# Kernel tuning notes

Hardware: AMD Instinct MI355X
Metric: run time of the kernel (lower is better)

## Reference

```python
import jax, jax.numpy as jnp
import numpy as np

B, C, H, W = 4, 64, 128, 128
KH, KW = 5, 5
PAD = 2
HEADS, DIM_HEAD = 8, 8


def setup_inputs() -> dict:
    key = jax.random.key(0)
    k1, k2, k3, k4 = jax.random.split(key, 4)
    return {
        "features1": jax.random.normal(k1, (B, C, H, W), dtype=jnp.float32),
        "features2": jax.random.normal(k2, (B, C, H, W), dtype=jnp.float32),
        "rel_h": jax.random.normal(k3, (C // 2, 1, 1, KH, 1), dtype=jnp.float32),
        "rel_w": jax.random.normal(k4, (C // 2, 1, 1, 1, KW), dtype=jnp.float32),
    }


def reference(features1, features2, rel_h, rel_w):
    b, c, h, w = features1.shape
    K = KH * KW
    # pad key/value source spatially
    padded = jnp.pad(features2, ((0, 0), (0, 0), (PAD, PAD), (PAD, PAD)))
    # materialize sliding windows: [B, C, H, W, KH*KW], kw index minor (matches torch unfold(2).unfold(3))
    windows = jnp.stack(
        [padded[:, :, i:i + h, j:j + w] for i in range(KH) for j in range(KW)],
        axis=-1,
    )
    # relative position bias: first C/2 channels get rel_h, last C/2 get rel_w
    relh = jnp.broadcast_to(rel_h.reshape(c // 2, KH, 1), (c // 2, KH, KW))
    relw = jnp.broadcast_to(rel_w.reshape(c // 2, 1, KW), (c // 2, KH, KW))
    rel = jnp.concatenate([relh, relw], axis=0).reshape(c, K)  # [C, K]
    k = windows + rel[None, :, None, None, :]
    v = windows
    q = features1.reshape(b, HEADS, DIM_HEAD, h, w, 1)
    k = k.reshape(b, HEADS, DIM_HEAD, h, w, K)
    v = v.reshape(b, HEADS, DIM_HEAD, h, w, K)
    # per-channel windowed softmax attention (no reduction over channel in scores)
    attn = jax.nn.softmax(q * k, axis=-1)
    # einsum 'abcdef,abcdef->acbde' from torch: output is [B, dim_head, heads, H, W]
    out = jnp.einsum('bhcxyk,bhcxyk->bchxy', attn, v)
    return out.reshape(b, c, h, w)
```

## Files before the change

### kernel.cpp

```cpp
#include <hip/hip_runtime.h>

#define B_ 4
#define C_ 64
#define H_ 128
#define W_ 128
#define R_ 4
#define NROWS (R_ + 4)
#define LOG2E 1.44269504088896340736f

template<int HALF>
__device__ __forceinline__ void sa_body(int x, int y0,
    const float* __restrict__ f1p, const float* __restrict__ f2p,
    const float* __restrict__ relp, float* __restrict__ outp)
{
    float rel5[5];
    #pragma unroll
    for (int k = 0; k < 5; ++k) rel5[k] = relp[k];

    int coff[5]; float msk[5];
    #pragma unroll
    for (int j = 0; j < 5; ++j) {
        const int kx = x + j - 2;
        coff[j] = kx < 0 ? 0 : (kx > W_ - 1 ? W_ - 1 : kx);
        msk[j]  = (kx >= 0 && kx < W_) ? 1.0f : 0.0f;
    }

    float w[NROWS][5];
    #pragma unroll
    for (int t = 0; t < NROWS; ++t) {
        const int ky = y0 + t - 2;
        if (ky >= 0 && ky < H_) {
            const float* rp = f2p + ky * W_;
            #pragma unroll
            for (int j = 0; j < 5; ++j) w[t][j] = rp[coff[j]];
        } else {
            #pragma unroll
            for (int j = 0; j < 5; ++j) w[t][j] = 0.0f;
        }
    }
    float qv[R_];
    #pragma unroll
    for (int r = 0; r < R_; ++r) qv[r] = f1p[(y0 + r) * W_ + x];

    #pragma unroll
    for (int t = 0; t < NROWS; ++t) {
        #pragma unroll
        for (int j = 0; j < 5; ++j) w[t][j] *= msk[j];
    }

    #pragma unroll
    for (int r = 0; r < R_; ++r) {
        const float q2 = qv[r] * LOG2E;
        float prel[5];
        #pragma unroll
        for (int k = 0; k < 5; ++k) prel[k] = q2 * rel5[k];

        float sum0 = 0.f, sum1 = 0.f, dot0 = 0.f, dot1 = 0.f;
        #pragma unroll
        for (int i = 0; i < 5; ++i) {
            #pragma unroll
            for (int j = 0; j < 5; ++j) {
                const float v  = w[r + i][j];
                const float sc = __builtin_fmaf(q2, v, prel[HALF == 0 ? i : j]);
                const float p  = __builtin_amdgcn_exp2f(sc);
                if (((i * 5 + j) & 1) == 0) { sum0 += p; dot0 = __builtin_fmaf(p, v, dot0); }
                else                        { sum1 += p; dot1 = __builtin_fmaf(p, v, dot1); }
            }
        }
        const float sum = sum0 + sum1;
        const float dot = dot0 + dot1;
        outp[(y0 + r) * W_ + x] = dot * __builtin_amdgcn_rcpf(sum);
    }
}

__global__ __launch_bounds__(256) void sa_kernel(
    const float* __restrict__ f1, const float* __restrict__ f2,
    const float* __restrict__ relh, const float* __restrict__ relw,
    float* __restrict__ out)
{
    const int tid   = threadIdx.x;
    const int x     = tid & (W_ - 1);
    const int s     = tid >> 7;
    const int blk   = blockIdx.x;
    const int spair = blk & (H_ / R_ / 2 - 1);
    const int bc    = blk >> 4;
    const int c     = bc & (C_ - 1);
    const int b     = bc >> 6;
    const int y0    = __builtin_amdgcn_readfirstlane((spair * 2 + s) * R_);

    const size_t img = (size_t)(b * C_ + c) * (H_ * W_);
    const float* f1p = f1 + img;
    const float* f2p = f2 + img;

    const int c_out = (c & 7) * 8 + (c >> 3);
    float* outp = out + (size_t)(b * C_ + c_out) * (H_ * W_);

    if (c < C_ / 2) sa_body<0>(x, y0, f1p, f2p, relh + c * 5, outp);
    else            sa_body<1>(x, y0, f1p, f2p, relw + (c - C_ / 2) * 5, outp);
}

extern "C" void kernel_launch(void* const* d_in, const int* in_sizes, int n_in,
                              void* d_out, int out_size, void* d_ws, size_t ws_size,
                              hipStream_t stream) {
    const float* f1   = (const float*)d_in[0];
    const float* f2   = (const float*)d_in[1];
    const float* relh = (const float*)d_in[2];
    const float* relw = (const float*)d_in[3];
    float* out = (float*)d_out;

    const int grid = B_ * C_ * (H_ / R_ / 2);
    sa_kernel<<<grid, 256, 0, stream>>>(f1, f2, relh, relw, out);
}
```

Measured before the change: 24.93 us.

## Compute 4x4 output tile per thread with float4 loads and packed v2f math

Each thread now computes a 4-wide by 4-tall output tile instead of a 1-wide column of 4 rows. It loads f2 rows as three float4 vectors into a rotating 5-row register buffer, reads q with a float4 load and writes output with a float4 store. It also uses 2-wide vector FMA types that may map to packed FP32 instructions. The aim is to cut redundant window loads and per-element load instructions and raise ALU throughput. The cost is higher register pressure, and the grid shrinks to 1024 blocks.

```diff
diff --git a/kernel.cpp b/kernel.cpp
--- a/kernel.cpp
+++ b/kernel.cpp
@@ -4,12 +4,16 @@
 #define C_ 64
 #define H_ 128
 #define W_ 128
-#define R_ 4
-#define NROWS (R_ + 4)
 #define LOG2E 1.44269504088896340736f
 
+typedef float v2f __attribute__((ext_vector_type(2)));
+
+__device__ __forceinline__ v2f exp2v(v2f x) {
+    return (v2f){ __builtin_amdgcn_exp2f(x.x), __builtin_amdgcn_exp2f(x.y) };
+}
+
 template<int HALF>
-__device__ __forceinline__ void sa_body(int x, int y0,
+__device__ __forceinline__ void sa_body(int x0, int y0,
     const float* __restrict__ f1p, const float* __restrict__ f2p,
     const float* __restrict__ relp, float* __restrict__ outp)
 {
@@ -17,59 +21,93 @@
     #pragma unroll
     for (int k = 0; k < 5; ++k) rel5[k] = relp[k];
 
-    int coff[5]; float msk[5];
-    #pragma unroll
-    for (int j = 0; j < 5; ++j) {
-        const int kx = x + j - 2;
-        coff[j] = kx < 0 ? 0 : (kx > W_ - 1 ? W_ - 1 : kx);
-        msk[j]  = (kx >= 0 && kx < W_) ? 1.0f : 0.0f;
-    }
+    const float mL = (x0 > 0) ? 1.0f : 0.0f;
+    const float mR = (x0 < W_ - 4) ? 1.0f : 0.0f;
+    const int eM = (x0 >= 4) ? x0 - 4 : 0;
+    const int eC = x0;
+    const int eP = (x0 <= W_ - 8) ? x0 + 4 : W_ - 4;
 
-    float w[NROWS][5];
-    #pragma unroll
-    for (int t = 0; t < NROWS; ++t) {
-        const int ky = y0 + t - 2;
-        if (ky >= 0 && ky < H_) {
-            const float* rp = f2p + ky * W_;
-            #pragma unroll
-            for (int j = 0; j < 5; ++j) w[t][j] = rp[coff[j]];
-        } else {
-            #pragma unroll
-            for (int j = 0; j < 5; ++j) w[t][j] = 0.0f;
-        }
-    }
-    float qv[R_];
-    #pragma unroll
-    for (int r = 0; r < R_; ++r) qv[r] = f1p[(y0 + r) * W_ + x];
+    float w[5][8];
+
+    auto load_row = [&](int slot, int ky) {
+        const int kycl = ky < 0 ? 0 : (ky > H_ - 1 ? H_ - 1 : ky);
+        const float rv = ((unsigned)ky < (unsigned)H_) ? 1.0f : 0.0f;
+        const float* rp = f2p + kycl * W_;
+        const float4 qm = *(const float4*)(rp + eM);
+        const float4 q0 = *(const float4*)(rp + eC);
+        const float4 qp = *(const float4*)(rp + eP);
+        const float mLr = mL * rv, mRr = mR * rv;
+        w[slot][0] = qm.z * mLr; w[slot][1] = qm.w * mLr;
+        w[slot][2] = q0.x * rv;  w[slot][3] = q0.y * rv;
+        w[slot][4] = q0.z * rv;  w[slot][5] = q0.w * rv;
+        w[slot][6] = qp.x * mRr; w[slot][7] = qp.y * mRr;
+    };
 
     #pragma unroll
-    for (int t = 0; t < NROWS; ++t) {
-        #pragma unroll
-        for (int j = 0; j < 5; ++j) w[t][j] *= msk[j];
-    }
+    for (int t = 0; t < 4; ++t) load_row(t, y0 + t - 2);
 
     #pragma unroll
-    for (int r = 0; r < R_; ++r) {
-        const float q2 = qv[r] * LOG2E;
-        float prel[5];
+    for (int r = 0; r < 4; ++r) {
+        load_row((r + 4) % 5, y0 + r + 2);
+
+        const float4 q4 = *(const float4*)(f1p + (y0 + r) * W_ + x0);
+        const float qs[4] = {q4.x, q4.y, q4.z, q4.w};
+        float res[4];
+
         #pragma unroll
-        for (int k = 0; k < 5; ++k) prel[k] = q2 * rel5[k];
+        for (int xo = 0; xo < 4; ++xo) {
+            const float q2 = qs[xo] * LOG2E;
+            const v2f q2v = {q2, q2};
 
-        float sum0 = 0.f, sum1 = 0.f, dot0 = 0.f, dot1 = 0.f;
-        #pragma unroll
-        for (int i = 0; i < 5; ++i) {
+            float pr[5];
             #pragma unroll
-            for (int j = 0; j < 5; ++j) {
-                const float v  = w[r + i][j];
-                const float sc = __builtin_fmaf(q2, v, prel[HALF == 0 ? i : j]);
-                const float p  = __builtin_amdgcn_exp2f(sc);
-                if (((i * 5 + j) & 1) == 0) { sum0 += p; dot0 = __builtin_fmaf(p, v, dot0); }
-                else                        { sum1 += p; dot1 = __builtin_fmaf(p, v, dot1); }
+            for (int k = 0; k < 5; ++k) pr[k] = q2 * rel5[k];
+            const v2f prA = {pr[0], pr[1]};
+            const v2f prB = {pr[2], pr[3]};
+            const float prC = pr[4];
+
+            v2f s0 = {0.f, 0.f}, s1 = {0.f, 0.f};
+            v2f d0 = {0.f, 0.f}, d1 = {0.f, 0.f};
+            float lv[5];
+
+            #pragma unroll
+            for (int i = 0; i < 5; ++i) {
+                const float* W8 = w[(r + i) % 5];
+                const v2f va = {W8[xo + 0], W8[xo + 1]};
+                const v2f vb = {W8[xo + 2], W8[xo + 3]};
+                const v2f pa = (HALF == 0) ? (v2f){pr[i], pr[i]} : prA;
+                const v2f pb = (HALF == 0) ? (v2f){pr[i], pr[i]} : prB;
+                const v2f p0 = exp2v(__builtin_elementwise_fma(va, q2v, pa));
+                s0 += p0; d0 = __builtin_elementwise_fma(p0, va, d0);
+                const v2f p1 = exp2v(__builtin_elementwise_fma(vb, q2v, pb));
+                s1 += p1; d1 = __builtin_elementwise_fma(p1, vb, d1);
+                lv[i] = W8[xo + 4];
             }
+            {
+                const v2f v = {lv[0], lv[1]};
+                const v2f pp = (HALF == 0) ? (v2f){pr[0], pr[1]} : (v2f){prC, prC};
+                const v2f p = exp2v(__builtin_elementwise_fma(v, q2v, pp));
+                s0 += p; d0 = __builtin_elementwise_fma(p, v, d0);
+            }
+            {
+                const v2f v = {lv[2], lv[3]};
+                const v2f pp = (HALF == 0) ? (v2f){pr[2], pr[3]} : (v2f){prC, prC};
+                const v2f p = exp2v(__builtin_elementwise_fma(v, q2v, pp));
+                s1 += p; d1 = __builtin_elementwise_fma(p, v, d1);
+            }
+            float ss, ds;
+            {
+                const float pp = (HALF == 0) ? pr[4] : prC;
+                const float p = __builtin_amdgcn_exp2f(__builtin_fmaf(q2, lv[4], pp));
+                ss = p; ds = p * lv[4];
+            }
+            const v2f st = s0 + s1, dt = d0 + d1;
+            const float sum = st.x + st.y + ss;
+            const float dot = dt.x + dt.y + ds;
+            res[xo] = dot * __builtin_amdgcn_rcpf(sum);
         }
-        const float sum = sum0 + sum1;
-        const float dot = dot0 + dot1;
-        outp[(y0 + r) * W_ + x] = dot * __builtin_amdgcn_rcpf(sum);
+
+        *(float4*)(outp + (y0 + r) * W_ + x0) = (float4){res[0], res[1], res[2], res[3]};
     }
 }
 
@@ -79,14 +117,15 @@
     float* __restrict__ out)
 {
     const int tid   = threadIdx.x;
-    const int x     = tid & (W_ - 1);
-    const int s     = tid >> 7;
+    const int xq    = tid & 31;
+    const int ys    = tid >> 5;
     const int blk   = blockIdx.x;
-    const int spair = blk & (H_ / R_ / 2 - 1);
-    const int bc    = blk >> 4;
+    const int chunk = blk & 3;
+    const int bc    = blk >> 2;
     const int c     = bc & (C_ - 1);
     const int b     = bc >> 6;
-    const int y0    = __builtin_amdgcn_readfirstlane((spair * 2 + s) * R_);
+    const int x0    = xq << 2;
+    const int y0    = chunk * 32 + ys * 4;
 
     const size_t img = (size_t)(b * C_ + c) * (H_ * W_);
     const float* f1p = f1 + img;
@@ -95,8 +134,8 @@
     const int c_out = (c & 7) * 8 + (c >> 3);
     float* outp = out + (size_t)(b * C_ + c_out) * (H_ * W_);
 
-    if (c < C_ / 2) sa_body<0>(x, y0, f1p, f2p, relh + c * 5, outp);
-    else            sa_body<1>(x, y0, f1p, f2p, relw + (c - C_ / 2) * 5, outp);
+    if (c < C_ / 2) sa_body<0>(x0, y0, f1p, f2p, relh + c * 5, outp);
+    else            sa_body<1>(x0, y0, f1p, f2p, relw + (c - C_ / 2) * 5, outp);
 }
 
 extern "C" void kernel_launch(void* const* d_in, const int* in_sizes, int n_in,
@@ -108,6 +147,6 @@
     const float* relw = (const float*)d_in[3];
     float* out = (float*)d_out;
 
-    const int grid = B_ * C_ * (H_ / R_ / 2);
+    const int grid = B_ * C_ * 4;
     sa_kernel<<<grid, 256, 0, stream>>>(f1, f2, relh, relw, out);
 }
```

New measurement: 21.65 us. 1.15x faster.
